# Kernel tuning notes

Measured on AMD Instinct MI355X. Metric: run time of the kernel, lower is better.

The kernel has to match this reference:

```python
import jax, jax.numpy as jnp
import numpy as np

SIZE = 128      # reconstruction grid (size x size)
ANGLES = 128    # number of projection angles after interpolation
B, C, H, W = 2, 8, 128, 128  # batch, channels, detector rows (z-slices), detector cols
N_VIEWS = 8


def setup_inputs() -> dict:
    key = jax.random.key(0)
    keys = jax.random.split(key, N_VIEWS)
    return {f"f{i}": jax.random.normal(keys[i], (B, C, H, W), dtype=jnp.float32)
            for i in range(N_VIEWS)}


def _fbp(projections, size, n_angles):
    # projections: (B, C, H, V, W) -- V stacked views, W detector columns
    b, c, h, v, w = projections.shape
    # Interpolation step: resize V views -> n_angles angles (linear, half-pixel,
    # matching F.interpolate default semantics)
    sino = jax.image.resize(projections, (b, c, h, n_angles, w), method="linear")
    # Ram-Lak ramp filter along the detector-column axis
    ramp = jnp.abs(jnp.fft.fftfreq(w)).astype(jnp.float32)
    filt = jnp.real(jnp.fft.ifft(jnp.fft.fft(sino, axis=-1) * ramp, axis=-1)).astype(sino.dtype)
    # Back-projection (parallel beam, per z-slice H)
    thetas = jnp.arange(n_angles, dtype=jnp.float32) * (jnp.pi / n_angles)
    xs = jnp.arange(size, dtype=jnp.float32) - (size - 1) / 2.0
    X, Y = jnp.meshgrid(xs, xs, indexing="xy")  # (S, S)
    center = (w - 1) / 2.0

    sino_per_angle = jnp.moveaxis(filt, 3, 0)  # (A, B, C, H, W)

    def body(acc, inputs):
        theta, sino_a = inputs                       # sino_a: (B, C, H, W)
        t = X * jnp.cos(theta) + Y * jnp.sin(theta) + center  # (S, S)
        t = jnp.clip(t, 0.0, w - 1.0)
        t0 = jnp.floor(t).astype(jnp.int32)
        t1 = jnp.minimum(t0 + 1, w - 1)
        w1 = (t - t0).astype(sino_a.dtype)
        v0 = sino_a[..., t0]                         # (B, C, H, S, S) gather
        v1 = sino_a[..., t1]
        acc = acc + v0 * (1.0 - w1) + v1 * w1
        return acc, None

    acc0 = jnp.zeros((b, c, h, size, size), dtype=sino.dtype)
    vol, _ = jax.lax.scan(body, acc0, (thetas, sino_per_angle))
    return vol * (jnp.pi / (2.0 * n_angles))


def reference(f0, f1, f2, f3, f4, f5, f6, f7):
    # torch.cat([f.unsqueeze(3) for f in features], dim=3) == stack on new axis 3
    projections = jnp.stack([f0, f1, f2, f3, f4, f5, f6, f7], axis=3)  # (B,C,H,V,W)
    return _fbp(projections, SIZE, ANGLES)
```

## Files before the change

kernel.cpp:

```cpp
#include <hip/hip_runtime.h>
#include <math.h>

#define W 128
#define NANG 128
#define SZ 128
#define NV 8
#define NROWS 2048
#define K_DIM 1024
#define NPIX 16384
#define OUT_SCALE 0.012271846303085130f

typedef _Float16 f16x8 __attribute__((ext_vector_type(8)));
typedef _Float16 f16x4 __attribute__((ext_vector_type(4)));
typedef float    f32x4 __attribute__((ext_vector_type(4)));

#define CF_OFF 4096
#define PF_OFF 36864
#define WV_OFF (36864 + (size_t)NROWS * K_DIM * 2)

struct Ptrs8 { const float* p[8]; };

__device__ __forceinline__ void glds16(const void* g, void* l) {
    __builtin_amdgcn_global_load_lds(
        (const __attribute__((address_space(1))) void*)g,
        (__attribute__((address_space(3))) void*)l, 16, 0, 0);
}

__global__ void k_tables(float* __restrict__ kt, float2* __restrict__ cs,
                         _Float16* __restrict__ cf) {
    __shared__ float kl[W];
    int d = threadIdx.x;
    const float w0 = 6.283185307179586f / (float)W * (float)d;
    float s = 0.f;
    for (int f = 1; f < 64; ++f)
        s = fmaf((float)f, __cosf(w0 * (float)f), s);
    s = 2.f * s + 64.f * ((d & 1) ? -1.f : 1.f);
    float kv = s * (1.f / (float)(W * W));
    kt[d] = kv;
    kl[d] = kv;
    float th = (float)d * ((float)M_PI / (float)NANG);
    cs[d] = make_float2(cosf(th), sinf(th));
    __syncthreads();
    for (int k = 0; k < W; ++k)
        cf[d * W + k] = (_Float16)kl[(d - k) & (W - 1)];
}

#define FS_A 136
__global__ __launch_bounds__(256)
void k_fgemm(Ptrs8 in, const _Float16* __restrict__ cf,
             _Float16* __restrict__ pf) {
    __shared__ _Float16 sA[64 * FS_A];
    __shared__ _Float16 sB[128 * FS_A];
    const int tid  = threadIdx.x;
    const int lane = tid & 63, wave = tid >> 6;
    const int fr = lane & 15, fg = lane >> 4;
    const int blk = blockIdx.x;

    {
        const int i   = tid >> 5;
        const int pos = (tid & 31) * 4;
#pragma unroll
        for (int v = 0; v < NV; ++v) {
            float4 x = *(const float4*)(in.p[v] + (size_t)(blk * 8 + i) * W + pos);
            f16x4 h = { (_Float16)x.x, (_Float16)x.y, (_Float16)x.z, (_Float16)x.w };
            *(f16x4*)&sA[(i * 8 + v) * FS_A + pos] = h;
        }
    }
#pragma unroll
    for (int j = 0; j < 8; ++j) {
        int c = tid + 256 * j;
        int n = c >> 4, kp = (c & 15) * 8;
        *(f16x8*)&sB[n * FS_A + kp] = *(const f16x8*)&cf[n * W + kp];
    }
    __syncthreads();

    f32x4 acc[8] = {};
#pragma unroll
    for (int kb = 0; kb < W; kb += 32) {
        f16x8 af = *(const f16x8*)&sA[(wave * 16 + fr) * FS_A + kb + fg * 8];
#pragma unroll
        for (int nt = 0; nt < 8; ++nt) {
            f16x8 bf = *(const f16x8*)&sB[(nt * 16 + fr) * FS_A + kb + fg * 8];
            acc[nt] = __builtin_amdgcn_mfma_f32_16x16x32_f16(af, bf, acc[nt], 0, 0, 0);
        }
    }
#pragma unroll
    for (int nt = 0; nt < 8; ++nt) {
        int m = blk * 64 + wave * 16 + fg * 4;
        int n = nt * 16 + fr;
#pragma unroll
        for (int rr = 0; rr < 4; ++rr)
            pf[(size_t)(m + rr) * W + n] = (_Float16)acc[nt][rr];
    }
}

__global__ void k_wv(const float2* __restrict__ cs, _Float16* __restrict__ wv) {
    __shared__ float wrow[8 * K_DIM];
    const int tid = threadIdx.x;
    const int p0 = blockIdx.x * 8;
    for (int i = tid; i < 8 * K_DIM; i += 256) wrow[i] = 0.f;
    __syncthreads();
    const int px  = tid >> 5;
    const int sub = tid & 31;
    const int p = p0 + px;
    const float x = (float)(p & 127) - 63.5f;
    const float y = (float)(p >> 7) - 63.5f;
    float* prow = &wrow[px * K_DIM];
    for (int a = sub; a < NANG; a += 32) {
        float2 c = cs[a];
        float t = fmaf(x, c.x, fmaf(y, c.y, 63.5f));
        t = fminf(fmaxf(t, 0.f), 127.f);
        float tf = fminf(floorf(t), 126.f);
        int   ti = (int)tf;
        float wt = t - tf;
        float src = ((float)a + 0.5f) * 0.0625f - 0.5f;
        src = fminf(fmaxf(src, 0.f), 7.f);
        float vf = floorf(src);
        int   v0 = (int)vf;
        int   v1 = v0 + 1 < NV ? v0 + 1 : NV - 1;
        float wa = src - vf;
        float wA0 = (1.f - wa) * OUT_SCALE;
        atomicAdd(&prow[v0 * W + ti],     wA0 * (1.f - wt));
        atomicAdd(&prow[v0 * W + ti + 1], wA0 * wt);
        if (v1 != v0) {
            float wA1 = wa * OUT_SCALE;
            atomicAdd(&prow[v1 * W + ti],     wA1 * (1.f - wt));
            atomicAdd(&prow[v1 * W + ti + 1], wA1 * wt);
        }
    }
    __syncthreads();
    uint* wvu = (uint*)(wv + (size_t)p0 * K_DIM);
#pragma unroll
    for (int j = 0; j < 16; ++j) {
        int j2 = tid + 256 * j;
        float2 w2 = *(const float2*)&wrow[j2 * 2];
        union { uint u; struct { _Float16 lo, hi; } h; } pk;
        pk.h.lo = (_Float16)w2.x; pk.h.hi = (_Float16)w2.y;
        wvu[j2] = pk.u;
    }
}

__global__ __launch_bounds__(256)
void k_gemm(const _Float16* __restrict__ A,
            const _Float16* __restrict__ B,
            float* __restrict__ out) {
    __shared__ _Float16 sA[128 * 32];
    __shared__ _Float16 sB[128 * 32];
    const int tid  = threadIdx.x;
    const int lane = tid & 63, wave = tid >> 6;
    const int m0 = blockIdx.y * 128;
    const int n0 = blockIdx.x * 128;
    const int wm = wave >> 1, wn = wave & 1;

    f32x4 acc[4][4] = {};

    const int c0 = wave * 64 + lane;
    const int c1 = c0 + 256;
    const _Float16* gA0 = A + (size_t)(m0 + (c0 >> 2)) * K_DIM + (c0 & 3) * 8;
    const _Float16* gA1 = A + (size_t)(m0 + (c1 >> 2)) * K_DIM + (c1 & 3) * 8;
    const _Float16* gB0 = B + (size_t)(n0 + (c0 >> 2)) * K_DIM + (c0 & 3) * 8;
    const _Float16* gB1 = B + (size_t)(n0 + (c1 >> 2)) * K_DIM + (c1 & 3) * 8;
    _Float16* lA0 = sA + wave * 512;
    _Float16* lA1 = sA + 2048 + wave * 512;
    _Float16* lB0 = sB + wave * 512;
    _Float16* lB1 = sB + 2048 + wave * 512;

    const int fr = lane & 15;
    const int fg = lane >> 4;

    for (int kb = 0; kb < K_DIM; kb += 32) {
        glds16(gA0 + kb, lA0);
        glds16(gA1 + kb, lA1);
        glds16(gB0 + kb, lB0);
        glds16(gB1 + kb, lB1);
        __syncthreads();
        f16x8 af[4], bf[4];
#pragma unroll
        for (int mt = 0; mt < 4; ++mt)
            af[mt] = *(const f16x8*)&sA[((wm * 4 + mt) * 16 + fr) * 32 + fg * 8];
#pragma unroll
        for (int nt = 0; nt < 4; ++nt)
            bf[nt] = *(const f16x8*)&sB[((wn * 4 + nt) * 16 + fr) * 32 + fg * 8];
#pragma unroll
        for (int mt = 0; mt < 4; ++mt)
#pragma unroll
            for (int nt = 0; nt < 4; ++nt)
                acc[mt][nt] = __builtin_amdgcn_mfma_f32_16x16x32_f16(
                    af[mt], bf[nt], acc[mt][nt], 0, 0, 0);
        __syncthreads();
    }

#pragma unroll
    for (int mt = 0; mt < 4; ++mt) {
#pragma unroll
        for (int nt = 0; nt < 4; ++nt) {
            int m = m0 + (wm * 4 + mt) * 16 + fg * 4;
            int n = n0 + (wn * 4 + nt) * 16 + fr;
            float* op = out + (size_t)m * NPIX + n;
#pragma unroll
            for (int rr = 0; rr < 4; ++rr)
                op[(size_t)rr * NPIX] = acc[mt][nt][rr];
        }
    }
}

extern "C" void kernel_launch(void* const* d_in, const int* in_sizes, int n_in,
                              void* d_out, int out_size, void* d_ws, size_t ws_size,
                              hipStream_t stream) {
    float*      kt = (float*)d_ws;
    float2*     cs = (float2*)((char*)d_ws + 512);
    _Float16*   cf = (_Float16*)((char*)d_ws + CF_OFF);
    _Float16*   pf = (_Float16*)((char*)d_ws + PF_OFF);
    _Float16*   wv = (_Float16*)((char*)d_ws + WV_OFF);

    Ptrs8 in;
    for (int i = 0; i < NV; ++i) in.p[i] = (const float*)d_in[i];

    k_tables<<<1, 128, 0, stream>>>(kt, cs, cf);
    k_fgemm<<<NROWS * NV / 64, 256, 0, stream>>>(in, cf, pf);
    k_wv<<<NPIX / 8, 256, 0, stream>>>(cs, wv);
    dim3 grid(NPIX / 128, NROWS / 128);
    k_gemm<<<grid, 256, 0, stream>>>(pf, wv, (float*)d_out);
}
```

Before: 294.5 us.

## Rewrite main GEMM as 256x256 double-buffered, swizzled, pipelined MFMA kernel

```diff
diff --git a/kernel.cpp b/kernel.cpp
--- a/kernel.cpp
+++ b/kernel.cpp
@@ -140,66 +140,161 @@
     }
 }
 
-__global__ __launch_bounds__(256)
+#define NT 16
+
+__device__ __forceinline__ void fencebar() {
+    asm volatile("" ::: "memory");
+    __builtin_amdgcn_s_barrier();
+    asm volatile("" ::: "memory");
+}
+
+__device__ __forceinline__ void stage_half(const _Float16* __restrict__ G, int R0,
+                                           int h, int kt, _Float16* L, int tid) {
+#pragma unroll
+    for (int r = 0; r < 2; ++r) {
+        const int c   = r * 512 + tid;
+        const int row = (h << 7) + (c >> 3);
+        const int q   = c & 7;
+        const _Float16* src = G + (size_t)(R0 + row) * K_DIM + kt * 64
+                                + ((q ^ (row & 7)) << 3);
+        _Float16* dst = L + (h << 13) + ((r * 512 + (tid & 448)) << 3);
+        glds16(src, dst);
+    }
+}
+
+__device__ __forceinline__ f16x8 frag(const _Float16* L, int row, int q) {
+    return *(const f16x8*)(L + row * 64 + ((q ^ (row & 7)) << 3));
+}
+
+__global__ __launch_bounds__(512, 2)
 void k_gemm(const _Float16* __restrict__ A,
-            const _Float16* __restrict__ B,
+            const _Float16* __restrict__ Bm,
             float* __restrict__ out) {
-    __shared__ _Float16 sA[128 * 32];
-    __shared__ _Float16 sB[128 * 32];
+    __shared__ _Float16 lds[65536];
     const int tid  = threadIdx.x;
-    const int lane = tid & 63, wave = tid >> 6;
-    const int m0 = blockIdx.y * 128;
-    const int n0 = blockIdx.x * 128;
-    const int wm = wave >> 1, wn = wave & 1;
-
-    f32x4 acc[4][4] = {};
-
-    const int c0 = wave * 64 + lane;
-    const int c1 = c0 + 256;
-    const _Float16* gA0 = A + (size_t)(m0 + (c0 >> 2)) * K_DIM + (c0 & 3) * 8;
-    const _Float16* gA1 = A + (size_t)(m0 + (c1 >> 2)) * K_DIM + (c1 & 3) * 8;
-    const _Float16* gB0 = B + (size_t)(n0 + (c0 >> 2)) * K_DIM + (c0 & 3) * 8;
-    const _Float16* gB1 = B + (size_t)(n0 + (c1 >> 2)) * K_DIM + (c1 & 3) * 8;
-    _Float16* lA0 = sA + wave * 512;
-    _Float16* lA1 = sA + 2048 + wave * 512;
-    _Float16* lB0 = sB + wave * 512;
-    _Float16* lB1 = sB + 2048 + wave * 512;
-
-    const int fr = lane & 15;
-    const int fg = lane >> 4;
-
-    for (int kb = 0; kb < K_DIM; kb += 32) {
-        glds16(gA0 + kb, lA0);
-        glds16(gA1 + kb, lA1);
-        glds16(gB0 + kb, lB0);
-        glds16(gB1 + kb, lB1);
-        __syncthreads();
-        f16x8 af[4], bf[4];
-#pragma unroll
-        for (int mt = 0; mt < 4; ++mt)
-            af[mt] = *(const f16x8*)&sA[((wm * 4 + mt) * 16 + fr) * 32 + fg * 8];
-#pragma unroll
-        for (int nt = 0; nt < 4; ++nt)
-            bf[nt] = *(const f16x8*)&sB[((wn * 4 + nt) * 16 + fr) * 32 + fg * 8];
-#pragma unroll
-        for (int mt = 0; mt < 4; ++mt)
-#pragma unroll
-            for (int nt = 0; nt < 4; ++nt)
-                acc[mt][nt] = __builtin_amdgcn_mfma_f32_16x16x32_f16(
-                    af[mt], bf[nt], acc[mt][nt], 0, 0, 0);
-        __syncthreads();
-    }
-
-#pragma unroll
-    for (int mt = 0; mt < 4; ++mt) {
-#pragma unroll
-        for (int nt = 0; nt < 4; ++nt) {
-            int m = m0 + (wm * 4 + mt) * 16 + fg * 4;
-            int n = n0 + (wn * 4 + nt) * 16 + fr;
+    const int lane = tid & 63, wid = tid >> 6;
+    const int wm = wid >> 2, wn = wid & 3;
+    const int fr = lane & 15, fg = lane >> 4;
+
+    const int flat = blockIdx.y * 64 + blockIdx.x;
+    const int swz  = (flat & 7) * 64 + (flat >> 3);
+    const int m0 = (swz >> 6) * 256;
+    const int n0 = (swz & 63) * 256;
+
+    _Float16* const A0 = lds;
+    _Float16* const B0 = lds + 16384;
+    _Float16* const A1 = lds + 32768;
+    _Float16* const B1 = lds + 49152;
+
+    stage_half(Bm, n0, 0, 0, B0, tid);
+    stage_half(A,  m0, 0, 0, A0, tid);
+    stage_half(Bm, n0, 1, 0, B0, tid);
+    stage_half(A,  m0, 1, 0, A0, tid);
+    stage_half(Bm, n0, 0, 1, B1, tid);
+    stage_half(A,  m0, 0, 1, A1, tid);
+    asm volatile("s_waitcnt vmcnt(4)" ::: "memory");
+    fencebar();
+
+    f32x4 acc[8][4] = {};
+    f16x8 af[4][2], bf[4][2];
+    const int ar = wm * 128 + fr;
+    const int br = wn * 64 + fr;
+
+    auto tile = [&](int t, _Float16* Ab, _Float16* Bb, _Float16* An, _Float16* Bn)
+        __attribute__((always_inline)) {
+#pragma unroll
+        for (int i = 0; i < 4; ++i) {
+            af[i][0] = frag(Ab, ar + i * 16, fg);
+            af[i][1] = frag(Ab, ar + i * 16, 4 + fg);
+        }
+#pragma unroll
+        for (int j = 0; j < 2; ++j) {
+            bf[j][0] = frag(Bb, br + j * 16, fg);
+            bf[j][1] = frag(Bb, br + j * 16, 4 + fg);
+        }
+        if (t + 1 < NT) stage_half(Bm, n0, 1, t + 1, Bn, tid);
+        fencebar();
+        asm volatile("s_waitcnt lgkmcnt(0)" ::: "memory");
+        __builtin_amdgcn_sched_barrier(0);
+        __builtin_amdgcn_s_setprio(1);
+#pragma unroll
+        for (int i = 0; i < 4; ++i)
+#pragma unroll
+            for (int j = 0; j < 2; ++j) {
+                acc[i][j] = __builtin_amdgcn_mfma_f32_16x16x32_f16(af[i][0], bf[j][0], acc[i][j], 0, 0, 0);
+                acc[i][j] = __builtin_amdgcn_mfma_f32_16x16x32_f16(af[i][1], bf[j][1], acc[i][j], 0, 0, 0);
+            }
+        __builtin_amdgcn_s_setprio(0);
+        fencebar();
+#pragma unroll
+        for (int j = 2; j < 4; ++j) {
+            bf[j][0] = frag(Bb, br + j * 16, fg);
+            bf[j][1] = frag(Bb, br + j * 16, 4 + fg);
+        }
+        if (t + 1 < NT) stage_half(A, m0, 1, t + 1, An, tid);
+        fencebar();
+        asm volatile("s_waitcnt lgkmcnt(0)" ::: "memory");
+        __builtin_amdgcn_sched_barrier(0);
+        __builtin_amdgcn_s_setprio(1);
+#pragma unroll
+        for (int i = 0; i < 4; ++i)
+#pragma unroll
+            for (int j = 2; j < 4; ++j) {
+                acc[i][j] = __builtin_amdgcn_mfma_f32_16x16x32_f16(af[i][0], bf[j][0], acc[i][j], 0, 0, 0);
+                acc[i][j] = __builtin_amdgcn_mfma_f32_16x16x32_f16(af[i][1], bf[j][1], acc[i][j], 0, 0, 0);
+            }
+        __builtin_amdgcn_s_setprio(0);
+        fencebar();
+#pragma unroll
+        for (int i = 0; i < 4; ++i) {
+            af[i][0] = frag(Ab, ar + 64 + i * 16, fg);
+            af[i][1] = frag(Ab, ar + 64 + i * 16, 4 + fg);
+        }
+        if (t + 2 < NT) stage_half(Bm, n0, 0, t + 2, Bb, tid);
+        fencebar();
+        asm volatile("s_waitcnt lgkmcnt(0)" ::: "memory");
+        __builtin_amdgcn_sched_barrier(0);
+        __builtin_amdgcn_s_setprio(1);
+#pragma unroll
+        for (int i = 0; i < 4; ++i)
+#pragma unroll
+            for (int j = 2; j < 4; ++j) {
+                acc[4 + i][j] = __builtin_amdgcn_mfma_f32_16x16x32_f16(af[i][0], bf[j][0], acc[4 + i][j], 0, 0, 0);
+                acc[4 + i][j] = __builtin_amdgcn_mfma_f32_16x16x32_f16(af[i][1], bf[j][1], acc[4 + i][j], 0, 0, 0);
+            }
+        __builtin_amdgcn_s_setprio(0);
+        fencebar();
+        if (t + 2 < NT) stage_half(A, m0, 0, t + 2, Ab, tid);
+        fencebar();
+        __builtin_amdgcn_s_setprio(1);
+#pragma unroll
+        for (int i = 0; i < 4; ++i)
+#pragma unroll
+            for (int j = 0; j < 2; ++j) {
+                acc[4 + i][j] = __builtin_amdgcn_mfma_f32_16x16x32_f16(af[i][0], bf[j][0], acc[4 + i][j], 0, 0, 0);
+                acc[4 + i][j] = __builtin_amdgcn_mfma_f32_16x16x32_f16(af[i][1], bf[j][1], acc[4 + i][j], 0, 0, 0);
+            }
+        __builtin_amdgcn_s_setprio(0);
+        if (t + 2 < NT)      asm volatile("s_waitcnt vmcnt(4)" ::: "memory");
+        else if (t + 1 < NT) asm volatile("s_waitcnt vmcnt(0)" ::: "memory");
+        fencebar();
+    };
+
+    for (int tt = 0; tt < NT; tt += 2) {
+        tile(tt,     A0, B0, A1, B1);
+        tile(tt + 1, A1, B1, A0, B0);
+    }
+
+#pragma unroll
+    for (int i = 0; i < 8; ++i) {
+#pragma unroll
+        for (int j = 0; j < 4; ++j) {
+            const int m = m0 + wm * 128 + i * 16 + fg * 4;
+            const int n = n0 + wn * 64 + j * 16 + fr;
             float* op = out + (size_t)m * NPIX + n;
 #pragma unroll
             for (int rr = 0; rr < 4; ++rr)
-                op[(size_t)rr * NPIX] = acc[mt][nt][rr];
+                op[(size_t)rr * NPIX] = acc[i][j][rr];
         }
     }
 }
@@ -219,6 +314,6 @@
     k_tables<<<1, 128, 0, stream>>>(kt, cs, cf);
     k_fgemm<<<NROWS * NV / 64, 256, 0, stream>>>(in, cf, pf);
     k_wv<<<NPIX / 8, 256, 0, stream>>>(cs, wv);
-    dim3 grid(NPIX / 128, NROWS / 128);
-    k_gemm<<<grid, 256, 0, stream>>>(pf, wv, (float*)d_out);
-}
+    dim3 grid(NPIX / 256, NROWS / 256);
+    k_gemm<<<grid, 512, 0, stream>>>(pf, wv, (float*)d_out);
+}
```

Result: faster. 263.3 us (-10.6%).
